# Performance work log

Hardware: AMD Instinct MI355X
Metric: run time of the kernel (lower is better)

The kernel has to match this reference:

```python
import jax, jax.numpy as jnp
import numpy as np

B = 1024        # query batch
M = 16384       # memory_size
D = 256         # feature_dim
A = (D // 8 + 1) * 8   # attention_dim = 264
H = 8           # num heads
DH = A // H     # head dim = 33


def setup_inputs() -> dict:
    key = jax.random.key(0)
    ks = jax.random.split(key, 16)
    s = 0.02
    return {
        "features": jax.random.normal(ks[0], (B, D), jnp.float32),
        "gradients": jax.random.normal(ks[1], (B, D), jnp.float32),
        "memory_keys": jax.random.normal(ks[2], (M, D), jnp.float32),
        "memory_values": jax.random.normal(ks[3], (M, D), jnp.float32),
        # feature_projector: Linear(D, A)
        "Wf": jax.random.normal(ks[4], (A, D), jnp.float32) * s,
        "bf": jnp.zeros((A,), jnp.float32),
        # MultiheadAttention in_proj (q, k, v), each Linear(A, A)
        "Wq": jax.random.normal(ks[5], (A, A), jnp.float32) * s,
        "Wk": jax.random.normal(ks[6], (A, A), jnp.float32) * s,
        "Wv": jax.random.normal(ks[7], (A, A), jnp.float32) * s,
        "bq": jnp.zeros((A,), jnp.float32),
        "bk": jnp.zeros((A,), jnp.float32),
        "bv": jnp.zeros((A,), jnp.float32),
        # MHA out_proj: Linear(A, A)
        "Wo": jax.random.normal(ks[8], (A, A), jnp.float32) * s,
        "bo": jnp.zeros((A,), jnp.float32),
        # output_projector: Linear(A, D)
        "Wout": jax.random.normal(ks[9], (D, A), jnp.float32) * s,
        "bout": jnp.zeros((D,), jnp.float32),
    }


def _forward(features, gradients, memory_keys, memory_values,
             Wf, bf, Wq, Wk, Wv, bq, bk, bv, Wo, bo, Wout, bout):
    # ---- compute_surprise: grad norm * min cdist(features, memory_keys) ----
    grad_mag = jnp.linalg.norm(gradients, axis=-1)                 # [B]
    f2 = jnp.sum(features * features, axis=-1, keepdims=True)      # [B,1]
    m2 = jnp.sum(memory_keys * memory_keys, axis=-1)               # [M]
    d2 = f2 + m2[None, :] - 2.0 * (features @ memory_keys.T)       # [B,M]
    dist = jnp.sqrt(jnp.maximum(d2, 0.0))
    min_dist = jnp.min(dist, axis=-1)                              # [B]
    surprise = grad_mag * min_dist                                 # [B]

    # ---- read_memory: project, MHA (q_len=1), output projection ----
    q = features @ Wf.T + bf          # [B,A]
    k = memory_keys @ Wf.T + bf       # [M,A]
    v = memory_values @ Wf.T + bf     # [M,A]

    qh = (q @ Wq.T + bq).reshape(B, H, DH)   # [B,H,DH]
    kh = (k @ Wk.T + bk).reshape(M, H, DH)   # [M,H,DH]
    vh = (v @ Wv.T + bv).reshape(M, H, DH)   # [M,H,DH]

    scale = 1.0 / jnp.sqrt(jnp.asarray(DH, qh.dtype))
    scores = jnp.einsum('bhd,mhd->bhm', qh, kh) * scale            # [B,H,M]
    attn = jax.nn.softmax(scores, axis=-1)
    ctx = jnp.einsum('bhm,mhd->bhd', attn, vh).reshape(B, A)       # [B,A]
    attn_out = ctx @ Wo.T + bo                                     # [B,A]
    retrieved = attn_out @ Wout.T + bout                           # [B,D]
    return retrieved, surprise


def reference(features, gradients, memory_keys, memory_values,
              Wf, bf, Wq, Wk, Wv, bq, bk, bv, Wo, bo, Wout, bout):
    return _forward(features, gradients, memory_keys, memory_values,
                    Wf, bf, Wq, Wk, Wv, bq, bk, bv, Wo, bo, Wout, bout)
```

## Files before the change

### kernel.cpp

```cpp
#include <hip/hip_runtime.h>
#include <math.h>

#define B_Q 1024
#define MEM 16384
#define DF  256
#define AD  264
#define NH  8
#define SPLIT 16
#define SCALE 0.17407765595569785f

typedef __attribute__((ext_vector_type(8)))  short bf16x8;
typedef __attribute__((ext_vector_type(4)))  float f32x4;
typedef __attribute__((ext_vector_type(16))) float f32x16;
typedef __attribute__((ext_vector_type(8)))  unsigned short u16x8;
typedef __attribute__((ext_vector_type(4)))  unsigned short u16x4;
typedef __fp16 fp16x2 __attribute__((ext_vector_type(2)));
typedef _Float16 f16x8 __attribute__((ext_vector_type(8)));

#define MFMA16(a,b,c)  __builtin_amdgcn_mfma_f32_16x16x32_bf16((a),(b),(c),0,0,0)
#define MFMA32(a,b,c)  __builtin_amdgcn_mfma_f32_32x32x16_bf16((a),(b),(c),0,0,0)
#define MFMA32H(a,b,c) __builtin_amdgcn_mfma_f32_32x32x16_f16((a),(b),(c),0,0,0)

__device__ __forceinline__ unsigned short f2bf(float x) {
  unsigned int u = __float_as_uint(x);
  return (unsigned short)((u + 0x7fffu + ((u >> 16) & 1u)) >> 16);
}
union uhw { fp16x2 h; unsigned u; };
__device__ __forceinline__ unsigned short f2h(float x) {
  uhw t; t.h = __builtin_amdgcn_cvt_pkrtz(x, x);
  return (unsigned short)(t.u & 0xFFFFu);
}
__device__ __forceinline__ unsigned pk_fma_f16(unsigned a, unsigned b, unsigned c) {
  unsigned d;
  asm("v_pk_fma_f16 %0, %1, %2, %3" : "=v"(d) : "v"(a), "v"(b), "v"(c));
  return d;
}
__device__ __forceinline__ void plswap(unsigned &x, unsigned &y) {
  asm volatile("v_permlane32_swap_b32 %0, %1" : "+v"(x), "+v"(y));
}
__device__ __forceinline__ void gload_lds16(const void* g, void* l) {
  __builtin_amdgcn_global_load_lds(
      (const __attribute__((address_space(1))) unsigned int*)g,
      (__attribute__((address_space(3))) unsigned int*)l, 16, 0, 0);
}

__global__ __launch_bounds__(256) void prelude_kernel(
    const float* __restrict__ f, const float* __restrict__ g,
    const float* __restrict__ k, const float* __restrict__ v,
    const float* __restrict__ Wq, const float* __restrict__ Wk,
    const float* __restrict__ Wv, const float* __restrict__ Wout,
    const float* __restrict__ Wf, const float* __restrict__ Wo,
    unsigned short* __restrict__ Fbf, unsigned short* __restrict__ Kbf,
    unsigned short* __restrict__ Vbf,
    float* __restrict__ f2, float* __restrict__ g2, float* __restrict__ m2,
    unsigned short* __restrict__ out6, float4* __restrict__ zreg)
{
  const int bid = blockIdx.x, t = threadIdx.x;
  if (bid < 4352) {
    zreg[bid*256 + t] = float4{0.f, 0.f, 0.f, 0.f};
  } else if (bid < 13056) {
    int gid = (bid - 4352) * 256 + t;
    int w = gid >> 6, lane = gid & 63;
    const float* src; unsigned short* dst; float* nrm; int row;
    if (w < 1024)       { row = w;         src = f + (size_t)row*DF; dst = Fbf + (size_t)row*DF; nrm = f2 + row; }
    else if (w < 2048)  { row = w - 1024;  src = g + (size_t)row*DF; dst = 0;                    nrm = g2 + row; }
    else if (w < 18432) { row = w - 2048;  src = k + (size_t)row*DF; dst = Kbf + (size_t)row*DF; nrm = m2 + row; }
    else                { row = w - 18432; src = v + (size_t)row*DF; dst = Vbf + (size_t)row*DF; nrm = 0; }
    float4 x = ((const float4*)src)[lane];
    if (dst) {
      u16x4 o; o[0]=f2bf(x.x); o[1]=f2bf(x.y); o[2]=f2bf(x.z); o[3]=f2bf(x.w);
      *(u16x4*)(dst + lane*4) = o;
    }
    if (nrm) {
      float s = x.x*x.x + x.y*x.y + x.z*x.z + x.w*x.w;
      #pragma unroll
      for (int off = 1; off < 64; off <<= 1) s += __shfl_xor(s, off, 64);
      if (lane == 0) *nrm = s;
    }
  } else {
    int gid = (bid - 13056) * 256 + t;
    if (gid >= 6*320*72) return;
    int arr = gid / (320*72);
    int rem = gid - arr*(320*72);
    int a = rem / 72;
    int c4 = (rem - a*72) * 4;
    u16x4 pk;
    #pragma unroll
    for (int i = 0; i < 4; ++i) {
      int c = c4 + i;
      float vv = 0.f;
      if (c < AD) {
        if (arr < 3)      { const float* s = arr==0?Wq:arr==1?Wk:Wv; if (a < AD) vv = s[a*AD + c]; }
        else if (arr == 3){ if (a < DF) vv = Wout[a*AD + c]; }
        else if (arr == 4){ if (a < DF) vv = Wf[c*DF + a]; }
        else              { if (a < AD) vv = Wo[c*AD + a]; }
      }
      pk[i] = f2bf(vv);
    }
    *(u16x4*)(out6 + (size_t)gid * 4) = pk;
  }
}

__global__ __launch_bounds__(256) void combine_kernel(
    const unsigned short* __restrict__ W6,
    const float* __restrict__ Wq, const float* __restrict__ Wk,
    const float* __restrict__ Wv, const float* __restrict__ Wout,
    const float* __restrict__ bf, const float* __restrict__ bq,
    const float* __restrict__ bk, const float* __restrict__ bv,
    const float* __restrict__ bo, const float* __restrict__ bout,
    unsigned short* __restrict__ WfQbf, unsigned short* __restrict__ WfKbf,
    unsigned short* __restrict__ WfVbf, unsigned short* __restrict__ Wco_b,
    float* __restrict__ bqp, float* __restrict__ bkp,
    float* __restrict__ bvp, float* __restrict__ bco)
{
  const float QS = SCALE * 1.4426950408889634f;
  const int bid = blockIdx.x;
  if (bid < 80) {
    const int seg = bid / 20, sub = bid % 20;
    int bm, bn; const unsigned short *X, *Wt;
    if (seg < 3) { bm = (sub >> 2)*64; bn = (sub & 3)*64;
                   X = W6 + (size_t)seg*320*288; Wt = W6 + (size_t)4*320*288; }
    else         { bm = (sub / 5)*64; bn = (sub % 5)*64;
                   X = W6 + (size_t)3*320*288; Wt = W6 + (size_t)5*320*288; }
    const int t = threadIdx.x, wid = t >> 6, lane = t & 63;
    const int lq = lane & 15, lg = lane >> 4;
    const int r0 = bm + wid*16;
    bf16x8 af[9];
    const unsigned short* arow = X + (size_t)(r0 + lq) * 288;
    #pragma unroll
    for (int c = 0; c < 9; ++c) af[c] = *(const bf16x8*)(arow + c*32 + lg*8);
    f32x4 acc[4] = {};
    #pragma unroll
    for (int c = 0; c < 9; ++c) {
      #pragma unroll
      for (int tt = 0; tt < 4; ++tt) {
        const unsigned short* brow = Wt + (size_t)(bn + tt*16 + lq) * 288;
        bf16x8 bw = *(const bf16x8*)(brow + c*32 + lg*8);
        acc[tt] = MFMA16(af[c], bw, acc[tt]);
      }
    }
    if (seg < 3) {
      unsigned short* Od = (seg == 0) ? WfQbf : (seg == 1) ? WfKbf : WfVbf;
      float sc = (seg == 0) ? QS : 1.0f;
      #pragma unroll
      for (int tt = 0; tt < 4; ++tt) {
        int col = bn + tt*16 + lq;
        #pragma unroll
        for (int j = 0; j < 4; ++j) {
          int row = r0 + lg*4 + j;
          if (row < AD) Od[row*256 + col] = f2bf(acc[tt][j] * sc);
        }
      }
    } else {
      #pragma unroll
      for (int tt = 0; tt < 4; ++tt) {
        int col = bn + tt*16 + lq;
        #pragma unroll
        for (int j = 0; j < 4; ++j) {
          int row = r0 + lg*4 + j;
          if (col < 288) Wco_b[row*288 + col] = (col < AD) ? f2bf(acc[tt][j]) : (unsigned short)0;
        }
      }
    }
  } else {
    int gw = (bid - 80) * 4 + (threadIdx.x >> 6);
    int lane = threadIdx.x & 63;
    const float* Wsrc; const float* vin; const float* badd; float* dst;
    int row; float sc = 1.0f;
    if (gw < 264)      { Wsrc = Wq;   vin = bf; badd = bq;   dst = bqp; row = gw;       sc = QS; }
    else if (gw < 528) { Wsrc = Wk;   vin = bf; badd = bk;   dst = bkp; row = gw - 264; }
    else if (gw < 792) { Wsrc = Wv;   vin = bf; badd = bv;   dst = bvp; row = gw - 528; }
    else               { Wsrc = Wout; vin = bo; badd = bout; dst = bco; row = gw - 792; }
    float s = 0.f;
    for (int c = lane; c < AD; c += 64) s = fmaf(Wsrc[row*AD + c], vin[c], s);
    #pragma unroll
    for (int off = 1; off < 64; off <<= 1) s += __shfl_xor(s, off, 64);
    if (lane == 0) dst[row] = (badd[row] + s) * sc;
  }
}

__global__ __launch_bounds__(256) void proj3_kernel(
    const unsigned short* __restrict__ Fbf, const unsigned short* __restrict__ Kbf,
    const unsigned short* __restrict__ Vbf,
    const unsigned short* __restrict__ WfQbf, const unsigned short* __restrict__ WfKbf,
    const unsigned short* __restrict__ WfVbf,
    const float* __restrict__ bqp, const float* __restrict__ bkp,
    const float* __restrict__ bvp,
    unsigned short* __restrict__ qh, unsigned short* __restrict__ kh,
    unsigned short* __restrict__ vhT)
{
  __shared__ unsigned short Wl[64*256];
  const int bid = blockIdx.x;
  const unsigned short *X, *W; const float* bias; unsigned short* out;
  int bx, by, R, transposed;
  if (bid < 40)       { X = Fbf; W = WfQbf; bias = bqp; out = qh;  R = B_Q; transposed = 0;
                        bx = bid % 8;           by = bid / 8; }
  else if (bid < 680) { X = Kbf; W = WfKbf; bias = bkp; out = kh;  R = MEM; transposed = 0;
                        bx = (bid - 40) % 128;  by = (bid - 40) / 128; }
  else                { X = Vbf; W = WfVbf; bias = bvp; out = vhT; R = MEM; transposed = 1;
                        bx = (bid - 680) % 128; by = (bid - 680) / 128; }
  const int t = threadIdx.x, wid = t >> 6, lane = t & 63;
  const int lq = lane & 15, lg = lane >> 4;
  const int a0 = by * 64;

  {
    const char* Bb = (const char*)W;
    int rowl = (lane >> 3);
    int cb  = (lane & 7) * 16;
    #pragma unroll
    for (int s = 0; s < 8; ++s) {
      int r = s*8 + rowl;
      gload_lds16(Bb + (size_t)(a0 + r)*512 + wid*128 + (cb ^ ((r & 7) << 4)),
                  (char*)Wl + (wid*8 + s)*1024);
    }
  }
  const int ar0 = bx * 128 + wid * 32;
  const unsigned short* arow0 = X + (size_t)(ar0 + lq) * 256 + lg*8;
  const unsigned short* arow1 = arow0 + 16*256;
  __syncthreads();

  f32x4 acc[2][4] = {};
  #pragma unroll
  for (int c = 0; c < 8; ++c) {
    bf16x8 a0f = *(const bf16x8*)(arow0 + c*32);
    bf16x8 a1f = *(const bf16x8*)(arow1 + c*32);
    #pragma unroll
    for (int tt = 0; tt < 4; ++tt) {
      int rb = tt*16 + lq;
      bf16x8 bw = *(const bf16x8*)((const char*)Wl + (c >> 1)*8192 + rb*128
                                   + (((c & 1)*64 + lg*16) ^ ((rb & 7) << 4)));
      acc[0][tt] = MFMA16(a0f, bw, acc[0][tt]);
      acc[1][tt] = MFMA16(a1f, bw, acc[1][tt]);
    }
  }
  #pragma unroll
  for (int tt = 0; tt < 4; ++tt) {
    int a = a0 + tt*16 + lq;
    if (a < AD) {
      int h = a / 33;
      int dh = a - h * 33;
      float bv = bias[a];
      #pragma unroll
      for (int i = 0; i < 2; ++i) {
        if (!transposed) {
          #pragma unroll
          for (int j = 0; j < 4; ++j) {
            int row = ar0 + i*16 + lg*4 + j;
            out[((size_t)h * R + row) * 64 + dh] = f2bf(acc[i][tt][j] + bv);
          }
        } else {
          u16x4 pk;
          #pragma unroll
          for (int j = 0; j < 4; ++j) pk[j] = f2h(acc[i][tt][j] + bv);
          *(u16x4*)(out + ((size_t)h * 48 + dh) * (size_t)MEM + ar0 + i*16 + lg*4) = pk;
        }
      }
    }
  }
}

__global__ __launch_bounds__(512) void fused_sa_kernel(
    const unsigned short* __restrict__ Fbf, const unsigned short* __restrict__ Kbf,
    const float* __restrict__ f2, const float* __restrict__ m2,
    float* __restrict__ pmin,
    const unsigned short* __restrict__ qh, const unsigned short* __restrict__ kh,
    const unsigned short* __restrict__ vhT,
    float* __restrict__ part_l, float* __restrict__ part_ctx)
{
  __shared__ unsigned short smem[64*256];
  const int id = blockIdx.x;
  const int t = threadIdx.x, wid = t >> 6, lane = t & 63;
  const int lq = lane & 15, lg = lane >> 4;

  if (id < 1024) {
    unsigned short* Bt = smem;
    const int bm = (id >> 8) * 256;
    const int bn = id & 255;
    const int bc = bn * 64;
    {
      const char* Bb = (const char*)Kbf;
      const int kchunk = wid >> 1, half = wid & 1;
      int rowl = (lane >> 3);
      int cb  = (lane & 7) * 16;
      #pragma unroll
      for (int s = 0; s < 4; ++s) {
        int r = half*32 + s*8 + rowl;
        gload_lds16(Bb + (size_t)(bc + r)*512 + kchunk*128 + (cb ^ ((r & 7) << 4)),
                    (char*)Bt + (kchunk*8 + half*4 + s)*1024);
      }
    }
    const int ar0 = bm + wid*32;
    const unsigned short* arow0 = Fbf + (size_t)(ar0 + lq) * 256 + lg*8;
    const unsigned short* arow1 = arow0 + 16*256;
    __syncthreads();
    f32x4 acc[2][4] = {};
    #pragma unroll
    for (int c = 0; c < 8; ++c) {
      bf16x8 a0 = *(const bf16x8*)(arow0 + c*32);
      bf16x8 a1 = *(const bf16x8*)(arow1 + c*32);
      #pragma unroll
      for (int tt = 0; tt < 4; ++tt) {
        int rb = tt*16 + lq;
        bf16x8 bw = *(const bf16x8*)((const char*)Bt + (c >> 1)*8192 + rb*128
                                     + (((c & 1)*64 + lg*16) ^ ((rb & 7) << 4)));
        acc[0][tt] = MFMA16(a0, bw, acc[0][tt]);
        acc[1][tt] = MFMA16(a1, bw, acc[1][tt]);
      }
    }
    #pragma unroll
    for (int i = 0; i < 2; ++i) {
      float rmin[4] = {1e30f, 1e30f, 1e30f, 1e30f};
      #pragma unroll
      for (int tt = 0; tt < 4; ++tt) {
        float m2c = m2[bc + tt*16 + lq];
        #pragma unroll
        for (int r = 0; r < 4; ++r) {
          float d2 = fmaxf(f2[ar0 + i*16 + lg*4 + r] + m2c - 2.0f*acc[i][tt][r], 0.f);
          rmin[r] = fminf(rmin[r], d2);
        }
      }
      #pragma unroll
      for (int off = 1; off < 16; off <<= 1)
        #pragma unroll
        for (int r = 0; r < 4; ++r) rmin[r] = fminf(rmin[r], __shfl_xor(rmin[r], off, 64));
      if (lq == 0) {
        #pragma unroll
        for (int r = 0; r < 4; ++r)
          pmin[(size_t)(ar0 + i*16 + lg*4 + r)*256 + bn] = rmin[r];
      }
    }
    return;
  }

  unsigned short* kt = smem;
  unsigned short* vt = smem + 8192;
  const int fid = id - 1024;
  const int l31 = lane & 31, lg2 = lane >> 5;
  const int qt = fid >> 7;
  const int pr = fid & 127;
  const int h = pr >> 4, sp = pr & 15;
  const int b0 = qt * 256;
  const int q  = b0 + wid*32 + l31;

  if (t < 64) ((unsigned*)(vt + 33*128))[t] = 0x3C003C00u;

  const unsigned c2u = 0x33B133B1u;
  const unsigned c1u = 0x398C398Cu;
  const unsigned oneu = 0x3C003C00u;
  auto p2 = [&](float a, float b) -> unsigned {
    uhw x; x.h = __builtin_amdgcn_cvt_pkrtz(a, b);
    unsigned tq = pk_fma_f16(x.u, c2u, c1u);
    return pk_fma_f16(x.u, tq, oneu);
  };

  bf16x8 qA[3];
  {
    const unsigned short* qrow = qh + ((size_t)h * B_Q + q) * 64;
    #pragma unroll
    for (int c = 0; c < 3; ++c) qA[c] = *(const bf16x8*)(qrow + c*16 + lg2*8);
  }

  f32x16 ctx0 = {}, ctx1 = {};
  const char* khb = (const char*)kh + (size_t)h * MEM * 128;
  const char* vhb = (const char*)vhT + (size_t)h * 48 * MEM * 2;
  const int m00 = sp * 1024;

  for (int it = 0; it < 8; ++it) {
    const int m0 = m00 + it * 128;
    __syncthreads();
    #pragma unroll
    for (int i = 0; i < 2; ++i) {
      int s = wid*2 + i;
      int row = s*8 + (lane >> 3);
      int cb  = (lane & 7) * 16;
      gload_lds16(khb + (size_t)(m0 + row)*128 + (cb ^ ((row & 7) << 4)),
                  (char*)kt + s*1024);
    }
    for (int s = wid; s < 9; s += 8) {
      int d  = s*4 + (lane >> 4);
      int cb = (lane & 15) * 16;
      if (d <= 32)
        gload_lds16(vhb + ((size_t)d * MEM + m0)*2 + (cb ^ ((d & 7) << 4)),
                    (char*)vt + s*1024);
    }
    __syncthreads();

    #pragma unroll
    for (int ms = 0; ms < 4; ++ms) {
      f32x16 s16 = {};
      {
        const char* krow = (const char*)kt + (ms*32 + l31)*128;
        #pragma unroll
        for (int c = 0; c < 3; ++c) {
          bf16x8 kb = *(const bf16x8*)(krow + ((c*32 + lg2*16) ^ ((l31 & 7) << 4)));
          s16 = MFMA32(kb, qA[c], s16);
        }
      }
      unsigned w0a = p2(s16[0],  s16[1]);
      unsigned w1a = p2(s16[2],  s16[3]);
      unsigned w2a = p2(s16[4],  s16[5]);
      unsigned w3a = p2(s16[6],  s16[7]);
      unsigned w0b = p2(s16[8],  s16[9]);
      unsigned w1b = p2(s16[10], s16[11]);
      unsigned w2b = p2(s16[12], s16[13]);
      unsigned w3b = p2(s16[14], s16[15]);
      plswap(w0a, w2a); plswap(w1a, w3a);
      plswap(w0b, w2b); plswap(w1b, w3b);
      union { unsigned u[4]; f16x8 v; } paA, paB;
      paA.u[0]=w0a; paA.u[1]=w1a; paA.u[2]=w2a; paA.u[3]=w3a;
      paB.u[0]=w0b; paB.u[1]=w1b; paB.u[2]=w2b; paB.u[3]=w3b;
      const char* vb = (const char*)vt;
      const int swd0 = ((l31 & 7) << 4);
      const int swd1 = (((32 + l31) & 7) << 4);
      {
        int cb = ms*64;
        f16x8 v0 = *(const f16x8*)(vb + l31*256        + ((cb + lg2*16) ^ swd0));
        f16x8 v1 = *(const f16x8*)(vb + (32+l31)*256   + ((cb + lg2*16) ^ swd1));
        ctx0 = MFMA32H(paA.v, v0, ctx0);
        ctx1 = MFMA32H(paA.v, v1, ctx1);
      }
      {
        int cb = ms*64 + 32;
        f16x8 v0 = *(const f16x8*)(vb + l31*256        + ((cb + lg2*16) ^ swd0));
        f16x8 v1 = *(const f16x8*)(vb + (32+l31)*256   + ((cb + lg2*16) ^ swd1));
        ctx0 = MFMA32H(paB.v, v0, ctx0);
        ctx1 = MFMA32H(paB.v, v1, ctx1);
      }
    }
  }
  #pragma unroll
  for (int r = 0; r < 16; ++r) {
    int ql = (r & 3) + 8*(r >> 2) + 4*lg2;
    int b  = b0 + wid*32 + ql;
    size_t pidx = (((size_t)b * NH) + h) * SPLIT + sp;
    part_ctx[pidx*33 + l31] = ctx0[r];
    if (l31 == 0) part_ctx[pidx*33 + 32] = ctx1[r];
    if (l31 == 1) part_l[pidx] = ctx1[r];
  }
}

__global__ __launch_bounds__(256) void combine2_kernel(
    const float* __restrict__ pl, const float* __restrict__ pc,
    unsigned short* __restrict__ ctxb,
    const float* __restrict__ pmin, const float* __restrict__ g2,
    float* __restrict__ out)
{
  const int bid = blockIdx.x;
  if (bid < 2048) {
    int w    = (bid * 256 + threadIdx.x) >> 6;
    int lane = threadIdx.x & 63;
    int b = w >> 3, h = w & 7;
    size_t base = (size_t)w * SPLIT;
    float L = 0.f;
    #pragma unroll
    for (int s = 0; s < SPLIT; ++s) L += pl[base+s];
    if (lane < 33) {
      float cv = 0.f;
      #pragma unroll
      for (int s = 0; s < SPLIT; ++s) cv += pc[(base+s)*33 + lane];
      ctxb[(size_t)b*288 + h*33 + lane] = f2bf(cv / L);
    } else if (h == 7 && lane < 57) {
      ctxb[(size_t)b*288 + 231 + lane] = 0;
    }
  } else {
    int row  = (bid - 2048) * 4 + (threadIdx.x >> 6);
    int lane = threadIdx.x & 63;
    float4 v = ((const float4*)(pmin + (size_t)row*256))[lane];
    float m = fminf(fminf(v.x, v.y), fminf(v.z, v.w));
    #pragma unroll
    for (int off = 1; off < 64; off <<= 1) m = fminf(m, __shfl_xor(m, off, 64));
    if (lane == 0)
      out[(size_t)B_Q * DF + row] = sqrtf(g2[row]) * sqrtf(fmaxf(m, 0.f));
  }
}

__global__ __launch_bounds__(256) void out_mfma_kernel(
    const unsigned short* __restrict__ ctxb, const unsigned short* __restrict__ Wco_b,
    const float* __restrict__ bco, float* __restrict__ out)
{
  const int t = threadIdx.x, wid = t >> 6, lane = t & 63;
  const int lq = lane & 15, lg = lane >> 4;
  const int r0 = blockIdx.x * 64 + wid * 16;
  const int d0 = blockIdx.y * 64;
  bf16x8 af[9];
  const unsigned short* arow = ctxb + (size_t)(r0 + lq) * 288;
  #pragma unroll
  for (int c = 0; c < 9; ++c) af[c] = *(const bf16x8*)(arow + c*32 + lg*8);
  f32x4 acc[4] = {};
  #pragma unroll
  for (int c = 0; c < 9; ++c) {
    #pragma unroll
    for (int tt = 0; tt < 4; ++tt) {
      const unsigned short* brow = Wco_b + (size_t)(d0 + tt*16 + lq) * 288;
      bf16x8 bw = *(const bf16x8*)(brow + c*32 + lg*8);
      acc[tt] = MFMA16(af[c], bw, acc[tt]);
    }
  }
  #pragma unroll
  for (int tt = 0; tt < 4; ++tt) {
    int d = d0 + tt*16 + lq;
    float bv = bco[d];
    #pragma unroll
    for (int j = 0; j < 4; ++j)
      out[(size_t)(r0 + lg*4 + j) * 256 + d] = acc[tt][j] + bv;
  }
}

extern "C" void kernel_launch(void* const* d_in, const int* in_sizes, int n_in,
                              void* d_out, int out_size, void* d_ws, size_t ws_size,
                              hipStream_t stream)
{
  const float* features  = (const float*)d_in[0];
  const float* gradients = (const float*)d_in[1];
  const float* keys      = (const float*)d_in[2];
  const float* values    = (const float*)d_in[3];
  const float* Wf   = (const float*)d_in[4];
  const float* bf   = (const float*)d_in[5];
  const float* Wq   = (const float*)d_in[6];
  const float* Wk   = (const float*)d_in[7];
  const float* Wv   = (const float*)d_in[8];
  const float* bq   = (const float*)d_in[9];
  const float* bk   = (const float*)d_in[10];
  const float* bv   = (const float*)d_in[11];
  const float* Wo   = (const float*)d_in[12];
  const float* bo   = (const float*)d_in[13];
  const float* Wout = (const float*)d_in[14];
  const float* bout = (const float*)d_in[15];
  float* out = (float*)d_out;
  (void)ws_size; (void)n_in; (void)in_sizes; (void)out_size;

  char* Wp = (char*)d_ws;
  size_t o = 0;
  auto alloc = [&](size_t bytes) -> void* {
    void* p = Wp + o; o = (o + bytes + 255) & ~(size_t)255; return p;
  };
  unsigned short* W6   = (unsigned short*)alloc((size_t)6*320*288*2);
  unsigned short* Wco_b= (unsigned short*)alloc((size_t)256*288*2);
  unsigned short* ctxb = (unsigned short*)alloc((size_t)B_Q*288*2);
  float* bqp   = (float*)alloc(320*4);
  float* bkp   = (float*)alloc(320*4);
  float* bvp   = (float*)alloc(320*4);
  float* bco   = (float*)alloc(320*4);
  float* f2    = (float*)alloc(B_Q*4);
  float* g2    = (float*)alloc(B_Q*4);
  float* m2    = (float*)alloc(MEM*4);
  float* pmin  = (float*)alloc((size_t)B_Q*256*4);
  float* part_l = (float*)alloc((size_t)B_Q*NH*SPLIT*4);
  float* part_ctx = (float*)alloc((size_t)B_Q*NH*SPLIT*33*4);
  unsigned short* Fbf = (unsigned short*)alloc((size_t)B_Q*DF*2);
  unsigned short* Kbf = (unsigned short*)alloc((size_t)MEM*DF*2);
  unsigned short* Vbf = (unsigned short*)alloc((size_t)MEM*DF*2);
  unsigned short* WfQbf = (unsigned short*)alloc((size_t)320*256*2);
  unsigned short* WfKbf = (unsigned short*)alloc((size_t)320*256*2);
  unsigned short* WfVbf = (unsigned short*)alloc((size_t)320*256*2);
  unsigned short* qh  = (unsigned short*)alloc((size_t)NH*B_Q*64*2);
  unsigned short* kh  = (unsigned short*)alloc((size_t)NH*MEM*64*2);
  unsigned short* vhT = (unsigned short*)alloc((size_t)NH*48*MEM*2);

  prelude_kernel<<<13596, 256, 0, stream>>>(
      features, gradients, keys, values, Wq, Wk, Wv, Wout, Wf, Wo,
      Fbf, Kbf, Vbf, f2, g2, m2, W6, (float4*)qh);
  combine_kernel<<<342, 256, 0, stream>>>(
      W6, Wq, Wk, Wv, Wout, bf, bq, bk, bv, bo, bout,
      WfQbf, WfKbf, WfVbf, Wco_b, bqp, bkp, bvp, bco);
  proj3_kernel<<<1320, 256, 0, stream>>>(
      Fbf, Kbf, Vbf, WfQbf, WfKbf, WfVbf, bqp, bkp, bvp, qh, kh, vhT);
  fused_sa_kernel<<<1536, 512, 0, stream>>>(
      Fbf, Kbf, f2, m2, pmin, qh, kh, vhT, part_l, part_ctx);
  combine2_kernel<<<2304, 256, 0, stream>>>(part_l, part_ctx, ctxb, pmin, g2, out);
  out_mfma_kernel<<<dim3(B_Q/64, DF/64), 256, 0, stream>>>(ctxb, Wco_b, bco, out);
}
```

Measured before the change: 105.9 us.

## Double-buffer K/V LDS tiles with prefetch and raise priority around MFMAs

The attention loop now uses two LDS buffers holding 64-row K and V tiles. The next tile is prefetched while the current one is computed, so each iteration needs one barrier instead of two and global-to-LDS latency overlaps with MFMA work. s_setprio is raised around the MFMA groups to favour matrix issue across waves. In exchange there are twice as many iterations, each with a smaller tile, and more barriers overall, and the V buffer uses a narrower row stride with a new swizzle that must stay correct.

```diff
diff --git a/kernel.cpp b/kernel.cpp
--- a/kernel.cpp
+++ b/kernel.cpp
@@ -332,8 +332,6 @@
     return;
   }
 
-  unsigned short* kt = smem;
-  unsigned short* vt = smem + 8192;
   const int fid = id - 1024;
   const int l31 = lane & 31, lg2 = lane >> 5;
   const int qt = fid >> 7;
@@ -342,7 +340,10 @@
   const int b0 = qt * 256;
   const int q  = b0 + wid*32 + l31;
 
-  if (t < 64) ((unsigned*)(vt + 33*128))[t] = 0x3C003C00u;
+  if (t < 64) {
+    int bb = t >> 5;
+    ((unsigned*)((char*)smem + 16384 + bb*8192 + 33*128))[t & 31] = 0x3C003C00u;
+  }
 
   const unsigned c2u = 0x33B133B1u;
   const unsigned c1u = 0x398C398Cu;
@@ -365,36 +366,41 @@
   const char* vhb = (const char*)vhT + (size_t)h * 48 * MEM * 2;
   const int m00 = sp * 1024;
 
-  for (int it = 0; it < 8; ++it) {
-    const int m0 = m00 + it * 128;
-    __syncthreads();
-    #pragma unroll
-    for (int i = 0; i < 2; ++i) {
-      int s = wid*2 + i;
-      int row = s*8 + (lane >> 3);
+  auto stageA = [&](int bb, int m0) {
+    {
+      int row = wid*8 + (lane >> 3);
       int cb  = (lane & 7) * 16;
       gload_lds16(khb + (size_t)(m0 + row)*128 + (cb ^ ((row & 7) << 4)),
-                  (char*)kt + s*1024);
-    }
-    for (int s = wid; s < 9; s += 8) {
-      int d  = s*4 + (lane >> 4);
-      int cb = (lane & 15) * 16;
+                  (char*)smem + bb*8192 + wid*1024);
+    }
+    if (wid < 5) {
+      int d  = wid*8 + (lane >> 3);
+      int cb = (lane & 7) * 16;
       if (d <= 32)
         gload_lds16(vhb + ((size_t)d * MEM + m0)*2 + (cb ^ ((d & 7) << 4)),
-                    (char*)vt + s*1024);
-    }
+                    (char*)smem + 16384 + bb*8192 + wid*1024);
+    }
+  };
+
+  stageA(0, m00);
+  for (int it = 0; it < 16; ++it) {
+    const int cur = it & 1;
     __syncthreads();
-
-    #pragma unroll
-    for (int ms = 0; ms < 4; ++ms) {
+    if (it < 15) stageA(cur ^ 1, m00 + (it + 1) * 64);
+    const char* ktb = (const char*)smem + cur*8192;
+    const char* vtb = (const char*)smem + 16384 + cur*8192;
+    #pragma unroll
+    for (int ms = 0; ms < 2; ++ms) {
       f32x16 s16 = {};
       {
-        const char* krow = (const char*)kt + (ms*32 + l31)*128;
+        const char* krow = ktb + (ms*32 + l31)*128;
+        __builtin_amdgcn_s_setprio(1);
         #pragma unroll
         for (int c = 0; c < 3; ++c) {
           bf16x8 kb = *(const bf16x8*)(krow + ((c*32 + lg2*16) ^ ((l31 & 7) << 4)));
           s16 = MFMA32(kb, qA[c], s16);
         }
+        __builtin_amdgcn_s_setprio(0);
       }
       unsigned w0a = p2(s16[0],  s16[1]);
       unsigned w1a = p2(s16[2],  s16[3]);
@@ -409,22 +415,19 @@
       union { unsigned u[4]; f16x8 v; } paA, paB;
       paA.u[0]=w0a; paA.u[1]=w1a; paA.u[2]=w2a; paA.u[3]=w3a;
       paB.u[0]=w0b; paB.u[1]=w1b; paB.u[2]=w2b; paB.u[3]=w3b;
-      const char* vb = (const char*)vt;
-      const int swd0 = ((l31 & 7) << 4);
-      const int swd1 = (((32 + l31) & 7) << 4);
+      const int swd = ((l31 & 7) << 4);
       {
         int cb = ms*64;
-        f16x8 v0 = *(const f16x8*)(vb + l31*256        + ((cb + lg2*16) ^ swd0));
-        f16x8 v1 = *(const f16x8*)(vb + (32+l31)*256   + ((cb + lg2*16) ^ swd1));
+        f16x8 v0 = *(const f16x8*)(vtb + l31*128      + ((cb + lg2*16) ^ swd));
+        f16x8 v1 = *(const f16x8*)(vtb + (32+l31)*128 + ((cb + lg2*16) ^ swd));
+        f16x8 v2 = *(const f16x8*)(vtb + l31*128      + ((cb + 32 + lg2*16) ^ swd));
+        f16x8 v3 = *(const f16x8*)(vtb + (32+l31)*128 + ((cb + 32 + lg2*16) ^ swd));
+        __builtin_amdgcn_s_setprio(1);
         ctx0 = MFMA32H(paA.v, v0, ctx0);
         ctx1 = MFMA32H(paA.v, v1, ctx1);
-      }
-      {
-        int cb = ms*64 + 32;
-        f16x8 v0 = *(const f16x8*)(vb + l31*256        + ((cb + lg2*16) ^ swd0));
-        f16x8 v1 = *(const f16x8*)(vb + (32+l31)*256   + ((cb + lg2*16) ^ swd1));
-        ctx0 = MFMA32H(paB.v, v0, ctx0);
-        ctx1 = MFMA32H(paB.v, v1, ctx1);
+        ctx0 = MFMA32H(paB.v, v2, ctx0);
+        ctx1 = MFMA32H(paB.v, v3, ctx1);
+        __builtin_amdgcn_s_setprio(0);
       }
     }
   }
```

Result: no change. 107.1 us (+1.2%).
